# Kernel optimization log

Hardware: AMD Instinct MI355X
Metric: run time of the kernel (lower is better)

The kernel has to match this reference:

```python
import jax, jax.numpy as jnp
import numpy as np

N = 100000   # nodes
E = 500000   # edges
IN = 256     # in_dim
H = 256      # mlp_hidden = gnn_hidden = out_hidden
R = 3        # num_relations
EPS = 1e-5   # BatchNorm eps


def _bn(x, g, b, m, v):
    # eval-mode BatchNorm1d with running stats (m, v)
    return (x - m) * g / jnp.sqrt(v + EPS) + b


def _rel_agg(feat_src, agg_idx, etype, n, r):
    # per-(node, relation) segment sum and count in one fused segment reduce
    sid = agg_idx * r + etype                                   # (E,)
    sums = jax.ops.segment_sum(feat_src, sid, num_segments=n * r).reshape(n, r, -1)
    cnt = jax.ops.segment_sum(jnp.ones(feat_src.shape[:1], feat_src.dtype), sid,
                              num_segments=n * r).reshape(n, r, 1)
    return sums, cnt


def _scre(x, row, col, etype, r):
    # x - mean over active relations of per-relation neighbor means (aggregated at row)
    n = x.shape[0]
    sums, cnt = _rel_agg(x[col], row, etype, n, r)
    means = sums / jnp.maximum(cnt, 1.0)                        # (n, r, f)
    rel_count = jnp.maximum(jnp.sum(jnp.minimum(cnt, 1.0), axis=1), 1.0)  # (n, 1)
    return x - jnp.sum(means, axis=1) / rel_count


def _rgcn(x, row, col, etype, w_rel, w_root, bias, r):
    # PyG RGCNConv (aggr='mean'): per-relation mean of source feats at target + root + bias
    n = x.shape[0]
    sums, cnt = _rel_agg(x[row], col, etype, n, r)
    means = sums / jnp.maximum(cnt, 1.0)                        # (n, r, f)
    return jnp.einsum('nrf,rfo->no', means, w_rel) + x @ w_root + bias


def _forward(x, edge_index, edge_type,
             mlp_w1, mlp_b1, mbn1_g, mbn1_b, mbn1_m, mbn1_v,
             mlp_w2, mlp_b2, mbn2_g, mbn2_b, mbn2_m, mbn2_v,
             r1_wrel, r1_wroot, r1_b, gbn1_g, gbn1_b, gbn1_m, gbn1_v,
             r2_wrel, r2_wroot, r2_b, gbn2_g, gbn2_b, gbn2_m, gbn2_v,
             out_w, out_b):
    row, col = edge_index[0], edge_index[1]
    # MLP branch (dropout off in eval)
    z = jax.nn.relu(_bn(x @ mlp_w1 + mlp_b1, mbn1_g, mbn1_b, mbn1_m, mbn1_v))
    z_mlp = jax.nn.relu(_bn(z @ mlp_w2 + mlp_b2, mbn2_g, mbn2_b, mbn2_m, mbn2_v))
    h = _scre(x, row, col, edge_type, R)
    z = jax.nn.relu(_bn(_rgcn(h, row, col, edge_type, r1_wrel, r1_wroot, r1_b, R),
                        gbn1_g, gbn1_b, gbn1_m, gbn1_v))
    z_gnn = jax.nn.relu(_bn(_rgcn(z, row, col, edge_type, r2_wrel, r2_wroot, r2_b, R),
                            gbn2_g, gbn2_b, gbn2_m, gbn2_v))
    z = jnp.concatenate([z_mlp, z_gnn], axis=-1)                # (N, 2H)
    return (z @ out_w + out_b)[:, 0]                            # logits (N,)


def setup_inputs() -> dict:
    key = jax.random.key(0)
    ks = jax.random.split(key, 16)

    def w(k, shape):
        return jax.random.normal(k, shape, jnp.float32) * 0.05

    inp = {
        'x': jax.random.normal(ks[0], (N, IN), jnp.float32),
        'edge_index': jax.random.randint(ks[1], (2, E), 0, N),
        'edge_type': jax.random.randint(ks[2], (E,), 0, R),
        # MLP branch
        'mlp_w1': w(ks[3], (IN, H)), 'mlp_b1': jnp.zeros((H,), jnp.float32),
        'mbn1_g': jnp.ones((H,), jnp.float32), 'mbn1_b': jnp.zeros((H,), jnp.float32),
        'mbn1_m': 0.01 * jax.random.normal(ks[4], (H,), jnp.float32),
        'mbn1_v': 1.0 + 0.1 * jax.random.uniform(ks[5], (H,), jnp.float32),
        'mlp_w2': w(ks[6], (H, H)), 'mlp_b2': jnp.zeros((H,), jnp.float32),
        'mbn2_g': jnp.ones((H,), jnp.float32), 'mbn2_b': jnp.zeros((H,), jnp.float32),
        'mbn2_m': 0.01 * jax.random.normal(ks[7], (H,), jnp.float32),
        'mbn2_v': 1.0 + 0.1 * jax.random.uniform(ks[8], (H,), jnp.float32),
        # RGCN layer 1
        'r1_wrel': w(ks[9], (R, IN, H)), 'r1_wroot': w(ks[10], (IN, H)),
        'r1_b': jnp.zeros((H,), jnp.float32),
        'gbn1_g': jnp.ones((H,), jnp.float32), 'gbn1_b': jnp.zeros((H,), jnp.float32),
        'gbn1_m': 0.01 * jax.random.normal(ks[11], (H,), jnp.float32),
        'gbn1_v': 1.0 + 0.1 * jax.random.uniform(ks[12], (H,), jnp.float32),
        # RGCN layer 2
        'r2_wrel': w(ks[13], (R, H, H)), 'r2_wroot': w(ks[14], (H, H)),
        'r2_b': jnp.zeros((H,), jnp.float32),
        'gbn2_g': jnp.ones((H,), jnp.float32), 'gbn2_b': jnp.zeros((H,), jnp.float32),
        'gbn2_m': 0.01 * jax.random.normal(ks[15], (H,), jnp.float32),
        'gbn2_v': 1.0 + 0.1 * jax.random.uniform(jax.random.fold_in(key, 99), (H,), jnp.float32),
        # output head (proj_head does not affect returned logits; omitted)
        'out_w': 0.05 * jax.random.normal(jax.random.fold_in(key, 100), (2 * H, 1), jnp.float32),
        'out_b': jnp.zeros((1,), jnp.float32),
    }
    return inp


def reference(x, edge_index, edge_type,
              mlp_w1, mlp_b1, mbn1_g, mbn1_b, mbn1_m, mbn1_v,
              mlp_w2, mlp_b2, mbn2_g, mbn2_b, mbn2_m, mbn2_v,
              r1_wrel, r1_wroot, r1_b, gbn1_g, gbn1_b, gbn1_m, gbn1_v,
              r2_wrel, r2_wroot, r2_b, gbn2_g, gbn2_b, gbn2_m, gbn2_v,
              out_w, out_b):
    return _forward(x, edge_index, edge_type,
                    mlp_w1, mlp_b1, mbn1_g, mbn1_b, mbn1_m, mbn1_v,
                    mlp_w2, mlp_b2, mbn2_g, mbn2_b, mbn2_m, mbn2_v,
                    r1_wrel, r1_wroot, r1_b, gbn1_g, gbn1_b, gbn1_m, gbn1_v,
                    r2_wrel, r2_wroot, r2_b, gbn2_g, gbn2_b, gbn2_m, gbn2_v,
                    out_w, out_b)
```

## Files before the change

### kernel.cpp

```cpp
#include <hip/hip_runtime.h>

#define BN_EPS 1e-5f

typedef unsigned short u16;
typedef short bf16x8 __attribute__((ext_vector_type(8)));
typedef float f32x4 __attribute__((ext_vector_type(4)));

__device__ __forceinline__ float bf2f(u16 u) {
    return __uint_as_float(((unsigned)u) << 16);
}
__device__ __forceinline__ u16 f2bf(float f) {
    unsigned u = __float_as_uint(f);
    u += 0x7FFFu + ((u >> 16) & 1u);
    return (u16)(u >> 16);
}

__global__ __launch_bounds__(256) void k_count(const int* __restrict__ ei,
                                               const int* __restrict__ et,
                                               int* __restrict__ cntR,
                                               int* __restrict__ cntRT,
                                               int* __restrict__ cntCT, int E) {
    int e = blockIdx.x * 256 + threadIdx.x;
    if (e >= E) return;
    int r = ei[e], c = ei[E + e], t = et[e];
    atomicAdd(cntR + r, 1);
    atomicAdd(cntRT + (size_t)r * 3 + t, 1);
    atomicAdd(cntCT + (size_t)c * 3 + t, 1);
}

__global__ __launch_bounds__(256) void k_scales(const int* __restrict__ cntRT,
                                                float* __restrict__ sc_r, int N) {
    int n = blockIdx.x * 256 + threadIdx.x;
    if (n >= N) return;
    int c0 = cntRT[n * 3 + 0], c1 = cntRT[n * 3 + 1], c2 = cntRT[n * 3 + 2];
    float relc = (float)((c0 > 0) + (c1 > 0) + (c2 > 0));
    if (relc < 1.f) relc = 1.f;
    sc_r[n * 3 + 0] = c0 > 0 ? 1.f / ((float)c0 * relc) : 0.f;
    sc_r[n * 3 + 1] = c1 > 0 ? 1.f / ((float)c1 * relc) : 0.f;
    sc_r[n * 3 + 2] = c2 > 0 ? 1.f / ((float)c2 * relc) : 0.f;
}

__global__ __launch_bounds__(256) void k_scan1(const int* __restrict__ in,
                                               int* __restrict__ out,
                                               int* __restrict__ bsums, int n) {
    __shared__ int sh[256];
    int t = threadIdx.x, base = blockIdx.x * 2048 + t * 8;
    int v[8];
    int s = 0;
#pragma unroll
    for (int j = 0; j < 8; ++j) {
        int idx = base + j;
        v[j] = idx < n ? in[idx] : 0;
        s += v[j];
    }
    sh[t] = s;
    __syncthreads();
    for (int off = 1; off < 256; off <<= 1) {
        int val = (t >= off) ? sh[t - off] : 0;
        __syncthreads();
        sh[t] += val;
        __syncthreads();
    }
    int run = sh[t] - s;
    if (t == 255) bsums[blockIdx.x] = sh[255];
#pragma unroll
    for (int j = 0; j < 8; ++j) {
        int idx = base + j;
        if (idx < n) out[idx] = run;
        run += v[j];
    }
}
__global__ __launch_bounds__(256) void k_scan2(int* __restrict__ bsums, int nb) {
    __shared__ int sh[256];
    int t = threadIdx.x;
    int v = t < nb ? bsums[t] : 0;
    sh[t] = v;
    __syncthreads();
    for (int off = 1; off < 256; off <<= 1) {
        int val = (t >= off) ? sh[t - off] : 0;
        __syncthreads();
        sh[t] += val;
        __syncthreads();
    }
    if (t < nb) bsums[t] = sh[t] - v;
}
__global__ __launch_bounds__(256) void k_scan3(int* __restrict__ out,
                                               const int* __restrict__ bsums, int n) {
    int i = blockIdx.x * 2048 + threadIdx.x * 8;
    int add = bsums[blockIdx.x];
#pragma unroll
    for (int j = 0; j < 8; ++j)
        if (i + j < n) out[i + j] += add;
}

__global__ __launch_bounds__(256) void k_scatter(const int* __restrict__ ei,
                                                 const int* __restrict__ et,
                                                 const float* __restrict__ sc_r,
                                                 const int* __restrict__ offR,
                                                 int* __restrict__ fillR,
                                                 int* __restrict__ idxR,
                                                 float* __restrict__ coefR,
                                                 const int* __restrict__ offC,
                                                 int* __restrict__ fillC,
                                                 int* __restrict__ idxC, int E) {
    int e = blockIdx.x * 256 + threadIdx.x;
    if (e >= E) return;
    int r = ei[e], c = ei[E + e], t = et[e];
    int pR = offR[r] + atomicAdd(fillR + r, 1);
    idxR[pR] = c;
    coefR[pR] = sc_r[(size_t)r * 3 + t];
    int key = c * 3 + t;
    int pC = offC[key] + atomicAdd(fillC + key, 1);
    idxC[pC] = r;
}

__global__ __launch_bounds__(256) void k_scre_gather(const float* __restrict__ x,
                                                     const int* __restrict__ idxR,
                                                     const float* __restrict__ coefR,
                                                     const int* __restrict__ offR,
                                                     const int* __restrict__ cntR,
                                                     u16* __restrict__ h, int N) {
    int node = blockIdx.x * 4 + (threadIdx.x >> 6);
    if (node >= N) return;
    int lane = threadIdx.x & 63;
    int start = offR[node], len = cntR[node];
    float4 acc = make_float4(0.f, 0.f, 0.f, 0.f);
    for (int i = 0; i < len; ++i) {
        int c = idxR[start + i];
        float s = coefR[start + i];
        float4 v = *reinterpret_cast<const float4*>(x + (size_t)c * 256 + lane * 4);
        acc.x += s * v.x;
        acc.y += s * v.y;
        acc.z += s * v.z;
        acc.w += s * v.w;
    }
    float4 xv = *reinterpret_cast<const float4*>(x + (size_t)node * 256 + lane * 4);
    ushort4 o;
    o.x = f2bf(xv.x - acc.x);
    o.y = f2bf(xv.y - acc.y);
    o.z = f2bf(xv.z - acc.z);
    o.w = f2bf(xv.w - acc.w);
    *reinterpret_cast<ushort4*>(h + (size_t)node * 256 + lane * 4) = o;
}

__global__ __launch_bounds__(256) void k_rgcn_gather(const u16* __restrict__ src,
                                                     const int* __restrict__ idxC,
                                                     const int* __restrict__ offC,
                                                     const int* __restrict__ cntC,
                                                     u16* __restrict__ means,
                                                     int s0, int s1) {
    int seg = s0 + blockIdx.x * 4 + (threadIdx.x >> 6);
    if (seg >= s1) return;
    int lane = threadIdx.x & 63;
    int start = offC[seg], len = cntC[seg];
    float4 acc = make_float4(0.f, 0.f, 0.f, 0.f);
    for (int i = 0; i < len; ++i) {
        int r = idxC[start + i];
        ushort4 v = *reinterpret_cast<const ushort4*>(src + (size_t)r * 256 + lane * 4);
        acc.x += bf2f(v.x);
        acc.y += bf2f(v.y);
        acc.z += bf2f(v.z);
        acc.w += bf2f(v.w);
    }
    float inv = len > 0 ? 1.f / (float)len : 0.f;
    ushort4 o;
    o.x = f2bf(acc.x * inv);
    o.y = f2bf(acc.y * inv);
    o.z = f2bf(acc.z * inv);
    o.w = f2bf(acc.w * inv);
    *reinterpret_cast<ushort4*>(means + (size_t)(seg - s0) * 256 + lane * 4) = o;
}

__global__ __launch_bounds__(256) void k_wt(const float* __restrict__ W,
                                            u16* __restrict__ Wt, int K) {
    __shared__ float tile[32][33];
    int kb = blockIdx.x * 32, nb = blockIdx.y * 32;
    int tx = threadIdx.x & 31, ty = threadIdx.x >> 5;
#pragma unroll
    for (int j = 0; j < 4; ++j) {
        int k = kb + ty + j * 8;
        tile[ty + j * 8][tx] = W[(size_t)k * 256 + nb + tx];
    }
    __syncthreads();
#pragma unroll
    for (int j = 0; j < 4; ++j) {
        int n = nb + ty + j * 8;
        Wt[(size_t)n * K + kb + tx] = f2bf(tile[tx][ty + j * 8]);
    }
}

#define LDK 40

template <int A1_F32>
__global__ __launch_bounds__(256) void k_gemm_mfma(
    const void* __restrict__ A1v, int K1, const u16* __restrict__ W1t,
    const u16* __restrict__ A2, int K2, const u16* __restrict__ W2t,
    const float* __restrict__ bias,
    const float* __restrict__ bng, const float* __restrict__ bnb,
    const float* __restrict__ bnm, const float* __restrict__ bnv,
    u16* __restrict__ out, int M) {
    __shared__ u16 Asm[128 * LDK];
    __shared__ u16 Bsm[128 * LDK];
    const int tid = threadIdx.x;
    const int lane = tid & 63;
    const int wid = tid >> 6;
    const int wr = wid >> 1, wc = wid & 1;
    const int m0 = blockIdx.x * 128, n0 = blockIdx.y * 128;
    const int frow = lane & 15, fk = (lane >> 4) * 8;

    f32x4 acc[4][4] = {};

    for (int pass = 0; pass < 2; ++pass) {
        const int K = pass ? K2 : K1;
        if (K == 0) continue;
        const u16* Wt = pass ? W2t : W1t;
        for (int k0 = 0; k0 < K; k0 += 32) {
            __syncthreads();
#pragma unroll
            for (int j = 0; j < 2; ++j) {
                int q = tid + 256 * j;
                int row = q >> 2, kc = (q & 3) * 8;
                int gm = m0 + row;
                bf16x8 av = {};
                if (gm < M) {
                    if (pass == 0 && A1_F32) {
                        const float* p = (const float*)A1v + (size_t)gm * K + k0 + kc;
#pragma unroll
                        for (int e2 = 0; e2 < 8; ++e2)
                            ((u16*)&av)[e2] = f2bf(p[e2]);
                    } else {
                        const u16* Ab = pass ? A2 : (const u16*)A1v;
                        av = *reinterpret_cast<const bf16x8*>(Ab + (size_t)gm * K + k0 + kc);
                    }
                }
                *reinterpret_cast<bf16x8*>(&Asm[row * LDK + kc]) = av;
                bf16x8 wv = *reinterpret_cast<const bf16x8*>(Wt + (size_t)(n0 + row) * K + k0 + kc);
                *reinterpret_cast<bf16x8*>(&Bsm[row * LDK + kc]) = wv;
            }
            __syncthreads();
            bf16x8 af[4], bf[4];
#pragma unroll
            for (int i = 0; i < 4; ++i) {
                af[i] = *reinterpret_cast<const bf16x8*>(&Asm[(wr * 64 + i * 16 + frow) * LDK + fk]);
                bf[i] = *reinterpret_cast<const bf16x8*>(&Bsm[(wc * 64 + i * 16 + frow) * LDK + fk]);
            }
#pragma unroll
            for (int i = 0; i < 4; ++i)
#pragma unroll
                for (int j2 = 0; j2 < 4; ++j2)
                    acc[i][j2] = __builtin_amdgcn_mfma_f32_16x16x32_bf16(af[i], bf[j2], acc[i][j2], 0, 0, 0);
        }
    }

    const int crow = (lane >> 4) * 4;
#pragma unroll
    for (int fj = 0; fj < 4; ++fj) {
        int col = n0 + wc * 64 + fj * 16 + frow;
        float g = bng[col] * rsqrtf(bnv[col] + BN_EPS);
        float be = bnb[col] + (bias[col] - bnm[col]) * g;
#pragma unroll
        for (int fi = 0; fi < 4; ++fi) {
#pragma unroll
            for (int j = 0; j < 4; ++j) {
                int row = m0 + wr * 64 + fi * 16 + crow + j;
                if (row < M) {
                    float y = acc[fi][fj][j] * g + be;
                    out[(size_t)row * 256 + col] = f2bf(y > 0.f ? y : 0.f);
                }
            }
        }
    }
}

__global__ __launch_bounds__(256) void k_head(const u16* __restrict__ zm,
                                              const u16* __restrict__ zg,
                                              const float* __restrict__ ow,
                                              const float* __restrict__ ob,
                                              float* __restrict__ out, int N) {
    int n = blockIdx.x * 4 + (threadIdx.x >> 6);
    if (n >= N) return;
    int lane = threadIdx.x & 63;
    ushort4 a = *reinterpret_cast<const ushort4*>(zm + (size_t)n * 256 + lane * 4);
    float4 w = *reinterpret_cast<const float4*>(ow + lane * 4);
    float s = bf2f(a.x) * w.x + bf2f(a.y) * w.y + bf2f(a.z) * w.z + bf2f(a.w) * w.w;
    ushort4 b = *reinterpret_cast<const ushort4*>(zg + (size_t)n * 256 + lane * 4);
    float4 w2 = *reinterpret_cast<const float4*>(ow + 256 + lane * 4);
    s += bf2f(b.x) * w2.x + bf2f(b.y) * w2.y + bf2f(b.z) * w2.z + bf2f(b.w) * w2.w;
#pragma unroll
    for (int off = 32; off > 0; off >>= 1) s += __shfl_down(s, off);
    if (lane == 0) out[n] = s + ob[0];
}

static inline size_t alignup(size_t x) { return (x + 255) & ~(size_t)255; }

extern "C" void kernel_launch(void* const* d_in, const int* in_sizes, int n_in,
                              void* d_out, int out_size, void* d_ws, size_t ws_size,
                              hipStream_t stream) {
    const float* x = (const float*)d_in[0];
    const int* ei = (const int*)d_in[1];
    const int* et = (const int*)d_in[2];
    const float* mlp_w1 = (const float*)d_in[3];
    const float* mlp_b1 = (const float*)d_in[4];
    const float* mbn1_g = (const float*)d_in[5];
    const float* mbn1_b = (const float*)d_in[6];
    const float* mbn1_m = (const float*)d_in[7];
    const float* mbn1_v = (const float*)d_in[8];
    const float* mlp_w2 = (const float*)d_in[9];
    const float* mlp_b2 = (const float*)d_in[10];
    const float* mbn2_g = (const float*)d_in[11];
    const float* mbn2_b = (const float*)d_in[12];
    const float* mbn2_m = (const float*)d_in[13];
    const float* mbn2_v = (const float*)d_in[14];
    const float* r1_wrel = (const float*)d_in[15];
    const float* r1_wroot = (const float*)d_in[16];
    const float* r1_b = (const float*)d_in[17];
    const float* gbn1_g = (const float*)d_in[18];
    const float* gbn1_b = (const float*)d_in[19];
    const float* gbn1_m = (const float*)d_in[20];
    const float* gbn1_v = (const float*)d_in[21];
    const float* r2_wrel = (const float*)d_in[22];
    const float* r2_wroot = (const float*)d_in[23];
    const float* r2_b = (const float*)d_in[24];
    const float* gbn2_g = (const float*)d_in[25];
    const float* gbn2_b = (const float*)d_in[26];
    const float* gbn2_m = (const float*)d_in[27];
    const float* gbn2_v = (const float*)d_in[28];
    const float* out_w = (const float*)d_in[29];
    const float* out_b = (const float*)d_in[30];

    const int N = in_sizes[0] / 256;
    const int E = in_sizes[2];

    size_t off = 0;
    auto take = [&](size_t bytes) {
        size_t o = off;
        off = alignup(off + bytes);
        return o;
    };
    char* base = (char*)d_ws;
    size_t zeroOff = take((size_t)N * 11 * 4);
    int* cntR = (int*)(base + zeroOff);
    int* cntRT = cntR + N;
    int* cntCT = cntRT + (size_t)N * 3;
    int* fillR = cntCT + (size_t)N * 3;
    int* fillC = fillR + N;
    int* offR = (int*)(base + take((size_t)N * 4));
    int* offC = (int*)(base + take((size_t)N * 3 * 4));
    int* bsums = (int*)(base + take(256 * 4));
    float* sc_r = (float*)(base + take((size_t)N * 3 * 4));
    int* idxR = (int*)(base + take((size_t)E * 4));
    float* coefR = (float*)(base + take((size_t)E * 4));
    int* idxC = (int*)(base + take((size_t)E * 4));
    u16* w1t = (u16*)(base + take((size_t)256 * 256 * 2));
    u16* w2t = (u16*)(base + take((size_t)256 * 256 * 2));
    u16* r1relt = (u16*)(base + take((size_t)256 * 768 * 2));
    u16* r1roott = (u16*)(base + take((size_t)256 * 256 * 2));
    u16* r2relt = (u16*)(base + take((size_t)256 * 768 * 2));
    u16* r2roott = (u16*)(base + take((size_t)256 * 256 * 2));
    u16* regA = (u16*)(base + take((size_t)N * 256 * 2));
    u16* regB = (u16*)(base + take((size_t)N * 256 * 2));
    u16* regC = (u16*)(base + take((size_t)N * 256 * 2));
    size_t chunkOff = off;
    size_t avail = (ws_size > chunkOff) ? ws_size - chunkOff : 0;
    size_t ncap = avail / ((size_t)768 * 2);
    if (ncap < 2048) {
        hipMemsetAsync(d_out, 0, (size_t)out_size * 4, stream);
        return;
    }
    int Nc = (int)((ncap < (size_t)N) ? ncap : (size_t)N);
    int nch = (N + Nc - 1) / Nc;
    Nc = (N + nch - 1) / nch;
    u16* CH = (u16*)(base + chunkOff);

    hipMemsetAsync(cntR, 0, (size_t)N * 11 * 4, stream);
    k_count<<<(E + 255) / 256, 256, 0, stream>>>(ei, et, cntR, cntRT, cntCT, E);
    k_scales<<<(N + 255) / 256, 256, 0, stream>>>(cntRT, sc_r, N);
    {
        int n1 = N, nb1 = (n1 + 2047) / 2048;
        k_scan1<<<nb1, 256, 0, stream>>>(cntR, offR, bsums, n1);
        k_scan2<<<1, 256, 0, stream>>>(bsums, nb1);
        k_scan3<<<nb1, 256, 0, stream>>>(offR, bsums, n1);
        int n2 = N * 3, nb2 = (n2 + 2047) / 2048;
        k_scan1<<<nb2, 256, 0, stream>>>(cntCT, offC, bsums, n2);
        k_scan2<<<1, 256, 0, stream>>>(bsums, nb2);
        k_scan3<<<nb2, 256, 0, stream>>>(offC, bsums, n2);
    }
    k_scatter<<<(E + 255) / 256, 256, 0, stream>>>(ei, et, sc_r, offR, fillR, idxR,
                                                   coefR, offC, fillC, idxC, E);

    k_wt<<<dim3(8, 8), 256, 0, stream>>>(mlp_w1, w1t, 256);
    k_wt<<<dim3(8, 8), 256, 0, stream>>>(mlp_w2, w2t, 256);
    k_wt<<<dim3(24, 8), 256, 0, stream>>>(r1_wrel, r1relt, 768);
    k_wt<<<dim3(8, 8), 256, 0, stream>>>(r1_wroot, r1roott, 256);
    k_wt<<<dim3(24, 8), 256, 0, stream>>>(r2_wrel, r2relt, 768);
    k_wt<<<dim3(8, 8), 256, 0, stream>>>(r2_wroot, r2roott, 256);

    {
        dim3 g((N + 127) / 128, 2);
        k_gemm_mfma<1><<<g, 256, 0, stream>>>(x, 256, w1t, nullptr, 0, nullptr,
                                              mlp_b1, mbn1_g, mbn1_b, mbn1_m, mbn1_v,
                                              regA, N);
        k_gemm_mfma<0><<<g, 256, 0, stream>>>(regA, 256, w2t, nullptr, 0, nullptr,
                                              mlp_b2, mbn2_g, mbn2_b, mbn2_m, mbn2_v,
                                              regB, N);
    }

    k_scre_gather<<<(N + 3) / 4, 256, 0, stream>>>(x, idxR, coefR, offR, cntR, regA, N);

    for (int ch = 0; ch < nch; ++ch) {
        int n0 = ch * Nc;
        int n1 = (n0 + Nc < N) ? n0 + Nc : N;
        int Mc = n1 - n0;
        int s0 = n0 * 3, s1 = n1 * 3;
        k_rgcn_gather<<<(s1 - s0 + 3) / 4, 256, 0, stream>>>(regA, idxC, offC, cntCT,
                                                             CH, s0, s1);
        dim3 g((Mc + 127) / 128, 2);
        k_gemm_mfma<0><<<g, 256, 0, stream>>>(CH, 768, r1relt,
                                              regA + (size_t)n0 * 256, 256, r1roott,
                                              r1_b, gbn1_g, gbn1_b, gbn1_m, gbn1_v,
                                              regC + (size_t)n0 * 256, Mc);
    }

    for (int ch = 0; ch < nch; ++ch) {
        int n0 = ch * Nc;
        int n1 = (n0 + Nc < N) ? n0 + Nc : N;
        int Mc = n1 - n0;
        int s0 = n0 * 3, s1 = n1 * 3;
        k_rgcn_gather<<<(s1 - s0 + 3) / 4, 256, 0, stream>>>(regC, idxC, offC, cntCT,
                                                             CH, s0, s1);
        dim3 g((Mc + 127) / 128, 2);
        k_gemm_mfma<0><<<g, 256, 0, stream>>>(CH, 768, r2relt,
                                              regC + (size_t)n0 * 256, 256, r2roott,
                                              r2_b, gbn2_g, gbn2_b, gbn2_m, gbn2_v,
                                              regA + (size_t)n0 * 256, Mc);
    }

    k_head<<<(N + 3) / 4, 256, 0, stream>>>(regB, regA, out_w, out_b, (float*)d_out, N);
}
```

Before: 1.038 ms.

## Widen GEMM tile to full 256 columns with double-buffered register prefetch

The MFMA GEMM now computes all 256 output columns per block instead of splitting N across two blocks, so the A tile (including the fp32-to-bf16 converted input) is loaded only once. The two-pass K loop is flattened into a single loop with register prefetch and double-buffered LDS to overlap global loads with MFMA work. The RGCN gather moves to 32 lanes per segment with 8-element bf16 vector loads. This raises accumulator registers (4x8 fragments) and LDS use, which may lower occupancy, and halves the number of GEMM blocks.

Measured after the change: 1.017 ms. Within noise of the previous version (-1.9%).

```diff
diff --git a/kernel.cpp b/kernel.cpp
--- a/kernel.cpp
+++ b/kernel.cpp
@@ -149,26 +149,22 @@
                                                      const int* __restrict__ cntC,
                                                      u16* __restrict__ means,
                                                      int s0, int s1) {
-    int seg = s0 + blockIdx.x * 4 + (threadIdx.x >> 6);
+    int seg = s0 + blockIdx.x * 8 + (threadIdx.x >> 5);
     if (seg >= s1) return;
-    int lane = threadIdx.x & 63;
+    int lane = threadIdx.x & 31;
     int start = offC[seg], len = cntC[seg];
-    float4 acc = make_float4(0.f, 0.f, 0.f, 0.f);
+    float acc[8] = {};
     for (int i = 0; i < len; ++i) {
         int r = idxC[start + i];
-        ushort4 v = *reinterpret_cast<const ushort4*>(src + (size_t)r * 256 + lane * 4);
-        acc.x += bf2f(v.x);
-        acc.y += bf2f(v.y);
-        acc.z += bf2f(v.z);
-        acc.w += bf2f(v.w);
+        bf16x8 v = *reinterpret_cast<const bf16x8*>(src + (size_t)r * 256 + lane * 8);
+#pragma unroll
+        for (int e = 0; e < 8; ++e) acc[e] += bf2f(((u16*)&v)[e]);
     }
     float inv = len > 0 ? 1.f / (float)len : 0.f;
-    ushort4 o;
-    o.x = f2bf(acc.x * inv);
-    o.y = f2bf(acc.y * inv);
-    o.z = f2bf(acc.z * inv);
-    o.w = f2bf(acc.w * inv);
-    *reinterpret_cast<ushort4*>(means + (size_t)(seg - s0) * 256 + lane * 4) = o;
+    bf16x8 o;
+#pragma unroll
+    for (int e = 0; e < 8; ++e) ((u16*)&o)[e] = f2bf(acc[e] * inv);
+    *reinterpret_cast<bf16x8*>(means + (size_t)(seg - s0) * 256 + lane * 8) = o;
 }
 
 __global__ __launch_bounds__(256) void k_wt(const float* __restrict__ W,
@@ -190,6 +186,7 @@
 }
 
 #define LDK 40
+#define BM 128
 
 template <int A1_F32>
 __global__ __launch_bounds__(256) void k_gemm_mfma(
@@ -199,63 +196,103 @@
     const float* __restrict__ bng, const float* __restrict__ bnb,
     const float* __restrict__ bnm, const float* __restrict__ bnv,
     u16* __restrict__ out, int M) {
-    __shared__ u16 Asm[128 * LDK];
-    __shared__ u16 Bsm[128 * LDK];
+    __shared__ u16 Asm[2][BM * LDK];
+    __shared__ u16 Bsm[2][256 * LDK];
     const int tid = threadIdx.x;
     const int lane = tid & 63;
     const int wid = tid >> 6;
     const int wr = wid >> 1, wc = wid & 1;
-    const int m0 = blockIdx.x * 128, n0 = blockIdx.y * 128;
+    const int m0 = blockIdx.x * BM;
     const int frow = lane & 15, fk = (lane >> 4) * 8;
-
-    f32x4 acc[4][4] = {};
-
-    for (int pass = 0; pass < 2; ++pass) {
-        const int K = pass ? K2 : K1;
-        if (K == 0) continue;
-        const u16* Wt = pass ? W2t : W1t;
-        for (int k0 = 0; k0 < K; k0 += 32) {
-            __syncthreads();
-#pragma unroll
-            for (int j = 0; j < 2; ++j) {
-                int q = tid + 256 * j;
-                int row = q >> 2, kc = (q & 3) * 8;
-                int gm = m0 + row;
-                bf16x8 av = {};
+    const int arow = tid >> 2;
+    const int achunk = (tid & 3) * 8;
+
+    const int nsteps = (K1 + K2) >> 5;
+
+    f32x4 acc[4][8] = {};
+    bf16x8 pa[2], pb[4];
+
+    {
+        const int kg = 0;
+#pragma unroll
+        for (int s = 0; s < 2; ++s) {
+            int gm = m0 + arow + 64 * s;
+            bf16x8 v = {};
+            if (gm < M) {
+                if (A1_F32) {
+                    const float* p = (const float*)A1v + (size_t)gm * K1 + kg + achunk;
+#pragma unroll
+                    for (int e = 0; e < 8; ++e) ((u16*)&v)[e] = f2bf(p[e]);
+                } else {
+                    v = *reinterpret_cast<const bf16x8*>((const u16*)A1v + (size_t)gm * K1 + kg + achunk);
+                }
+            }
+            pa[s] = v;
+        }
+#pragma unroll
+        for (int s = 0; s < 4; ++s)
+            pb[s] = *reinterpret_cast<const bf16x8*>(W1t + (size_t)(arow + 64 * s) * K1 + kg + achunk);
+    }
+
+    int cur = 0;
+    for (int ks = 0; ks < nsteps; ++ks) {
+#pragma unroll
+        for (int s = 0; s < 2; ++s)
+            *reinterpret_cast<bf16x8*>(&Asm[cur][(arow + 64 * s) * LDK + achunk]) = pa[s];
+#pragma unroll
+        for (int s = 0; s < 4; ++s)
+            *reinterpret_cast<bf16x8*>(&Bsm[cur][(arow + 64 * s) * LDK + achunk]) = pb[s];
+        __syncthreads();
+
+        if (ks + 1 < nsteps) {
+            const int kg = (ks + 1) * 32;
+#pragma unroll
+            for (int s = 0; s < 2; ++s) {
+                int gm = m0 + arow + 64 * s;
+                bf16x8 v = {};
                 if (gm < M) {
-                    if (pass == 0 && A1_F32) {
-                        const float* p = (const float*)A1v + (size_t)gm * K + k0 + kc;
-#pragma unroll
-                        for (int e2 = 0; e2 < 8; ++e2)
-                            ((u16*)&av)[e2] = f2bf(p[e2]);
+                    if (kg < K1) {
+                        if (A1_F32) {
+                            const float* p = (const float*)A1v + (size_t)gm * K1 + kg + achunk;
+#pragma unroll
+                            for (int e = 0; e < 8; ++e) ((u16*)&v)[e] = f2bf(p[e]);
+                        } else {
+                            v = *reinterpret_cast<const bf16x8*>((const u16*)A1v + (size_t)gm * K1 + kg + achunk);
+                        }
                     } else {
-                        const u16* Ab = pass ? A2 : (const u16*)A1v;
-                        av = *reinterpret_cast<const bf16x8*>(Ab + (size_t)gm * K + k0 + kc);
+                        v = *reinterpret_cast<const bf16x8*>(A2 + (size_t)gm * K2 + (kg - K1) + achunk);
                     }
                 }
-                *reinterpret_cast<bf16x8*>(&Asm[row * LDK + kc]) = av;
-                bf16x8 wv = *reinterpret_cast<const bf16x8*>(Wt + (size_t)(n0 + row) * K + k0 + kc);
-                *reinterpret_cast<bf16x8*>(&Bsm[row * LDK + kc]) = wv;
+                pa[s] = v;
             }
-            __syncthreads();
-            bf16x8 af[4], bf[4];
-#pragma unroll
-            for (int i = 0; i < 4; ++i) {
-                af[i] = *reinterpret_cast<const bf16x8*>(&Asm[(wr * 64 + i * 16 + frow) * LDK + fk]);
-                bf[i] = *reinterpret_cast<const bf16x8*>(&Bsm[(wc * 64 + i * 16 + frow) * LDK + fk]);
+#pragma unroll
+            for (int s = 0; s < 4; ++s) {
+                int row = arow + 64 * s;
+                if (kg < K1)
+                    pb[s] = *reinterpret_cast<const bf16x8*>(W1t + (size_t)row * K1 + kg + achunk);
+                else
+                    pb[s] = *reinterpret_cast<const bf16x8*>(W2t + (size_t)row * K2 + (kg - K1) + achunk);
             }
+        }
+
+        bf16x8 af[4];
+#pragma unroll
+        for (int i = 0; i < 4; ++i)
+            af[i] = *reinterpret_cast<const bf16x8*>(&Asm[cur][(wr * 64 + i * 16 + frow) * LDK + fk]);
+#pragma unroll
+        for (int j = 0; j < 8; ++j) {
+            bf16x8 bfr = *reinterpret_cast<const bf16x8*>(&Bsm[cur][(wc * 128 + j * 16 + frow) * LDK + fk]);
 #pragma unroll
             for (int i = 0; i < 4; ++i)
-#pragma unroll
-                for (int j2 = 0; j2 < 4; ++j2)
-                    acc[i][j2] = __builtin_amdgcn_mfma_f32_16x16x32_bf16(af[i], bf[j2], acc[i][j2], 0, 0, 0);
+                acc[i][j] = __builtin_amdgcn_mfma_f32_16x16x32_bf16(af[i], bfr, acc[i][j], 0, 0, 0);
         }
+        cur ^= 1;
     }
 
     const int crow = (lane >> 4) * 4;
 #pragma unroll
-    for (int fj = 0; fj < 4; ++fj) {
-        int col = n0 + wc * 64 + fj * 16 + frow;
+    for (int fj = 0; fj < 8; ++fj) {
+        int col = wc * 128 + fj * 16 + frow;
         float g = bng[col] * rsqrtf(bnv[col] + BN_EPS);
         float be = bnb[col] + (bias[col] - bnm[col]) * g;
 #pragma unroll
@@ -396,7 +433,7 @@
     k_wt<<<dim3(8, 8), 256, 0, stream>>>(r2_wroot, r2roott, 256);
 
     {
-        dim3 g((N + 127) / 128, 2);
+        dim3 g((N + 127) / 128);
         k_gemm_mfma<1><<<g, 256, 0, stream>>>(x, 256, w1t, nullptr, 0, nullptr,
                                               mlp_b1, mbn1_g, mbn1_b, mbn1_m, mbn1_v,
                                               regA, N);
@@ -412,9 +449,9 @@
         int n1 = (n0 + Nc < N) ? n0 + Nc : N;
         int Mc = n1 - n0;
         int s0 = n0 * 3, s1 = n1 * 3;
-        k_rgcn_gather<<<(s1 - s0 + 3) / 4, 256, 0, stream>>>(regA, idxC, offC, cntCT,
+        k_rgcn_gather<<<(s1 - s0 + 7) / 8, 256, 0, stream>>>(regA, idxC, offC, cntCT,
                                                              CH, s0, s1);
-        dim3 g((Mc + 127) / 128, 2);
+        dim3 g((Mc + 127) / 128);
         k_gemm_mfma<0><<<g, 256, 0, stream>>>(CH, 768, r1relt,
                                               regA + (size_t)n0 * 256, 256, r1roott,
                                               r1_b, gbn1_g, gbn1_b, gbn1_m, gbn1_v,
@@ -426,9 +463,9 @@
         int n1 = (n0 + Nc < N) ? n0 + Nc : N;
         int Mc = n1 - n0;
         int s0 = n0 * 3, s1 = n1 * 3;
-        k_rgcn_gather<<<(s1 - s0 + 3) / 4, 256, 0, stream>>>(regC, idxC, offC, cntCT,
+        k_rgcn_gather<<<(s1 - s0 + 7) / 8, 256, 0, stream>>>(regC, idxC, offC, cntCT,
                                                              CH, s0, s1);
-        dim3 g((Mc + 127) / 128, 2);
+        dim3 g((Mc + 127) / 128);
         k_gemm_mfma<0><<<g, 256, 0, stream>>>(CH, 768, r2relt,
                                               regC + (size_t)n0 * 256, 256, r2roott,
                                               r2_b, gbn2_g, gbn2_b, gbn2_m, gbn2_v,
```

## Pre-convert x to bf16, widen gather vectors, and hoist GEMM global loads

Applied to the files above, without the earlier changes.

Adds a kernel that converts x to bf16 once. The first MLP GEMM and the SCRE gather then read bf16 instead of fp32, which halves the gather traffic on x. Both gather kernels switch to 32 lanes per row with 8-element (16-byte) loads and handle 8 rows per block. The GEMM now issues its global loads into registers before the barrier and writes them to LDS afterwards, so load latency overlaps the wait. SCRE now works on bf16-rounded x, which may change accuracy slightly, and the extra pass and buffer add memory traffic and workspace.

New measurement: 879.6 us. -15.2%, faster.

```diff
diff --git a/kernel.cpp b/kernel.cpp
--- a/kernel.cpp
+++ b/kernel.cpp
@@ -13,6 +13,24 @@
     unsigned u = __float_as_uint(f);
     u += 0x7FFFu + ((u >> 16) & 1u);
     return (u16)(u >> 16);
+}
+
+__global__ __launch_bounds__(256) void k_xbf(const float* __restrict__ x,
+                                             u16* __restrict__ xb, int n8) {
+    int i = blockIdx.x * 256 + threadIdx.x;
+    if (i >= n8) return;
+    const float4 a = *reinterpret_cast<const float4*>(x + (size_t)i * 8);
+    const float4 b = *reinterpret_cast<const float4*>(x + (size_t)i * 8 + 4);
+    bf16x8 o;
+    ((u16*)&o)[0] = f2bf(a.x);
+    ((u16*)&o)[1] = f2bf(a.y);
+    ((u16*)&o)[2] = f2bf(a.z);
+    ((u16*)&o)[3] = f2bf(a.w);
+    ((u16*)&o)[4] = f2bf(b.x);
+    ((u16*)&o)[5] = f2bf(b.y);
+    ((u16*)&o)[6] = f2bf(b.z);
+    ((u16*)&o)[7] = f2bf(b.w);
+    *reinterpret_cast<bf16x8*>(xb + (size_t)i * 8) = o;
 }
 
 __global__ __launch_bounds__(256) void k_count(const int* __restrict__ ei,
@@ -114,33 +132,29 @@
     idxC[pC] = r;
 }
 
-__global__ __launch_bounds__(256) void k_scre_gather(const float* __restrict__ x,
+__global__ __launch_bounds__(256) void k_scre_gather(const u16* __restrict__ xb,
                                                      const int* __restrict__ idxR,
                                                      const float* __restrict__ coefR,
                                                      const int* __restrict__ offR,
                                                      const int* __restrict__ cntR,
                                                      u16* __restrict__ h, int N) {
-    int node = blockIdx.x * 4 + (threadIdx.x >> 6);
+    int node = blockIdx.x * 8 + (threadIdx.x >> 5);
     if (node >= N) return;
-    int lane = threadIdx.x & 63;
+    int lane = threadIdx.x & 31;
     int start = offR[node], len = cntR[node];
-    float4 acc = make_float4(0.f, 0.f, 0.f, 0.f);
+    float acc[8] = {};
     for (int i = 0; i < len; ++i) {
         int c = idxR[start + i];
         float s = coefR[start + i];
-        float4 v = *reinterpret_cast<const float4*>(x + (size_t)c * 256 + lane * 4);
-        acc.x += s * v.x;
-        acc.y += s * v.y;
-        acc.z += s * v.z;
-        acc.w += s * v.w;
-    }
-    float4 xv = *reinterpret_cast<const float4*>(x + (size_t)node * 256 + lane * 4);
-    ushort4 o;
-    o.x = f2bf(xv.x - acc.x);
-    o.y = f2bf(xv.y - acc.y);
-    o.z = f2bf(xv.z - acc.z);
-    o.w = f2bf(xv.w - acc.w);
-    *reinterpret_cast<ushort4*>(h + (size_t)node * 256 + lane * 4) = o;
+        bf16x8 v = *reinterpret_cast<const bf16x8*>(xb + (size_t)c * 256 + lane * 8);
+#pragma unroll
+        for (int e = 0; e < 8; ++e) acc[e] += s * bf2f(((u16*)&v)[e]);
+    }
+    bf16x8 xv = *reinterpret_cast<const bf16x8*>(xb + (size_t)node * 256 + lane * 8);
+    bf16x8 o;
+#pragma unroll
+    for (int e = 0; e < 8; ++e) ((u16*)&o)[e] = f2bf(bf2f(((u16*)&xv)[e]) - acc[e]);
+    *reinterpret_cast<bf16x8*>(h + (size_t)node * 256 + lane * 8) = o;
 }
 
 __global__ __launch_bounds__(256) void k_rgcn_gather(const u16* __restrict__ src,
@@ -149,26 +163,22 @@
                                                      const int* __restrict__ cntC,
                                                      u16* __restrict__ means,
                                                      int s0, int s1) {
-    int seg = s0 + blockIdx.x * 4 + (threadIdx.x >> 6);
+    int seg = s0 + blockIdx.x * 8 + (threadIdx.x >> 5);
     if (seg >= s1) return;
-    int lane = threadIdx.x & 63;
+    int lane = threadIdx.x & 31;
     int start = offC[seg], len = cntC[seg];
-    float4 acc = make_float4(0.f, 0.f, 0.f, 0.f);
+    float acc[8] = {};
     for (int i = 0; i < len; ++i) {
         int r = idxC[start + i];
-        ushort4 v = *reinterpret_cast<const ushort4*>(src + (size_t)r * 256 + lane * 4);
-        acc.x += bf2f(v.x);
-        acc.y += bf2f(v.y);
-        acc.z += bf2f(v.z);
-        acc.w += bf2f(v.w);
+        bf16x8 v = *reinterpret_cast<const bf16x8*>(src + (size_t)r * 256 + lane * 8);
+#pragma unroll
+        for (int e = 0; e < 8; ++e) acc[e] += bf2f(((u16*)&v)[e]);
     }
     float inv = len > 0 ? 1.f / (float)len : 0.f;
-    ushort4 o;
-    o.x = f2bf(acc.x * inv);
-    o.y = f2bf(acc.y * inv);
-    o.z = f2bf(acc.z * inv);
-    o.w = f2bf(acc.w * inv);
-    *reinterpret_cast<ushort4*>(means + (size_t)(seg - s0) * 256 + lane * 4) = o;
+    bf16x8 o;
+#pragma unroll
+    for (int e = 0; e < 8; ++e) ((u16*)&o)[e] = f2bf(acc[e] * inv);
+    *reinterpret_cast<bf16x8*>(means + (size_t)(seg - s0) * 256 + lane * 8) = o;
 }
 
 __global__ __launch_bounds__(256) void k_wt(const float* __restrict__ W,
@@ -191,9 +201,8 @@
 
 #define LDK 40
 
-template <int A1_F32>
 __global__ __launch_bounds__(256) void k_gemm_mfma(
-    const void* __restrict__ A1v, int K1, const u16* __restrict__ W1t,
+    const u16* __restrict__ A1, int K1, const u16* __restrict__ W1t,
     const u16* __restrict__ A2, int K2, const u16* __restrict__ W2t,
     const float* __restrict__ bias,
     const float* __restrict__ bng, const float* __restrict__ bnb,
@@ -213,42 +222,41 @@
     for (int pass = 0; pass < 2; ++pass) {
         const int K = pass ? K2 : K1;
         if (K == 0) continue;
+        const u16* A = pass ? A2 : A1;
         const u16* Wt = pass ? W2t : W1t;
         for (int k0 = 0; k0 < K; k0 += 32) {
-            __syncthreads();
+            bf16x8 av[2], wv[2];
 #pragma unroll
             for (int j = 0; j < 2; ++j) {
                 int q = tid + 256 * j;
                 int row = q >> 2, kc = (q & 3) * 8;
                 int gm = m0 + row;
-                bf16x8 av = {};
-                if (gm < M) {
-                    if (pass == 0 && A1_F32) {
-                        const float* p = (const float*)A1v + (size_t)gm * K + k0 + kc;
-#pragma unroll
-                        for (int e2 = 0; e2 < 8; ++e2)
-                            ((u16*)&av)[e2] = f2bf(p[e2]);
-                    } else {
-                        const u16* Ab = pass ? A2 : (const u16*)A1v;
-                        av = *reinterpret_cast<const bf16x8*>(Ab + (size_t)gm * K + k0 + kc);
-                    }
-                }
-                *reinterpret_cast<bf16x8*>(&Asm[row * LDK + kc]) = av;
-                bf16x8 wv = *reinterpret_cast<const bf16x8*>(Wt + (size_t)(n0 + row) * K + k0 + kc);
-                *reinterpret_cast<bf16x8*>(&Bsm[row * LDK + kc]) = wv;
+                bf16x8 v = {};
+                if (gm < M)
+                    v = *reinterpret_cast<const bf16x8*>(A + (size_t)gm * K + k0 + kc);
+                av[j] = v;
+                wv[j] = *reinterpret_cast<const bf16x8*>(Wt + (size_t)(n0 + row) * K + k0 + kc);
             }
             __syncthreads();
-            bf16x8 af[4], bf[4];
+#pragma unroll
+            for (int j = 0; j < 2; ++j) {
+                int q = tid + 256 * j;
+                int row = q >> 2, kc = (q & 3) * 8;
+                *reinterpret_cast<bf16x8*>(&Asm[row * LDK + kc]) = av[j];
+                *reinterpret_cast<bf16x8*>(&Bsm[row * LDK + kc]) = wv[j];
+            }
+            __syncthreads();
+            bf16x8 af[4], bfr[4];
 #pragma unroll
             for (int i = 0; i < 4; ++i) {
                 af[i] = *reinterpret_cast<const bf16x8*>(&Asm[(wr * 64 + i * 16 + frow) * LDK + fk]);
-                bf[i] = *reinterpret_cast<const bf16x8*>(&Bsm[(wc * 64 + i * 16 + frow) * LDK + fk]);
+                bfr[i] = *reinterpret_cast<const bf16x8*>(&Bsm[(wc * 64 + i * 16 + frow) * LDK + fk]);
             }
 #pragma unroll
             for (int i = 0; i < 4; ++i)
 #pragma unroll
                 for (int j2 = 0; j2 < 4; ++j2)
-                    acc[i][j2] = __builtin_amdgcn_mfma_f32_16x16x32_bf16(af[i], bf[j2], acc[i][j2], 0, 0, 0);
+                    acc[i][j2] = __builtin_amdgcn_mfma_f32_16x16x32_bf16(af[i], bfr[j2], acc[i][j2], 0, 0, 0);
         }
     }
 
@@ -357,6 +365,7 @@
     u16* r1roott = (u16*)(base + take((size_t)256 * 256 * 2));
     u16* r2relt = (u16*)(base + take((size_t)256 * 768 * 2));
     u16* r2roott = (u16*)(base + take((size_t)256 * 256 * 2));
+    u16* xb = (u16*)(base + take((size_t)N * 256 * 2));
     u16* regA = (u16*)(base + take((size_t)N * 256 * 2));
     u16* regB = (u16*)(base + take((size_t)N * 256 * 2));
     u16* regC = (u16*)(base + take((size_t)N * 256 * 2));
@@ -371,6 +380,8 @@
     int nch = (N + Nc - 1) / Nc;
     Nc = (N + nch - 1) / nch;
     u16* CH = (u16*)(base + chunkOff);
+
+    k_xbf<<<(N * 32 + 255) / 256, 256, 0, stream>>>(x, xb, N * 32);
 
     hipMemsetAsync(cntR, 0, (size_t)N * 11 * 4, stream);
     k_count<<<(E + 255) / 256, 256, 0, stream>>>(ei, et, cntR, cntRT, cntCT, E);
@@ -397,28 +408,28 @@
 
     {
         dim3 g((N + 127) / 128, 2);
-        k_gemm_mfma<1><<<g, 256, 0, stream>>>(x, 256, w1t, nullptr, 0, nullptr,
-                                              mlp_b1, mbn1_g, mbn1_b, mbn1_m, mbn1_v,
-                                              regA, N);
-        k_gemm_mfma<0><<<g, 256, 0, stream>>>(regA, 256, w2t, nullptr, 0, nullptr,
-                                              mlp_b2, mbn2_g, mbn2_b, mbn2_m, mbn2_v,
-                                              regB, N);
-    }
-
-    k_scre_gather<<<(N + 3) / 4, 256, 0, stream>>>(x, idxR, coefR, offR, cntR, regA, N);
+        k_gemm_mfma<<<g, 256, 0, stream>>>(xb, 256, w1t, nullptr, 0, nullptr,
+                                           mlp_b1, mbn1_g, mbn1_b, mbn1_m, mbn1_v,
+                                           regA, N);
+        k_gemm_mfma<<<g, 256, 0, stream>>>(regA, 256, w2t, nullptr, 0, nullptr,
+                                           mlp_b2, mbn2_g, mbn2_b, mbn2_m, mbn2_v,
+                                           regB, N);
+    }
+
+    k_scre_gather<<<(N + 7) / 8, 256, 0, stream>>>(xb, idxR, coefR, offR, cntR, regA, N);
 
     for (int ch = 0; ch < nch; ++ch) {
         int n0 = ch * Nc;
         int n1 = (n0 + Nc < N) ? n0 + Nc : N;
         int Mc = n1 - n0;
         int s0 = n0 * 3, s1 = n1 * 3;
-        k_rgcn_gather<<<(s1 - s0 + 3) / 4, 256, 0, stream>>>(regA, idxC, offC, cntCT,
+        k_rgcn_gather<<<(s1 - s0 + 7) / 8, 256, 0, stream>>>(regA, idxC, offC, cntCT,
                                                              CH, s0, s1);
         dim3 g((Mc + 127) / 128, 2);
-        k_gemm_mfma<0><<<g, 256, 0, stream>>>(CH, 768, r1relt,
-                                              regA + (size_t)n0 * 256, 256, r1roott,
-                                              r1_b, gbn1_g, gbn1_b, gbn1_m, gbn1_v,
-                                              regC + (size_t)n0 * 256, Mc);
+        k_gemm_mfma<<<g, 256, 0, stream>>>(CH, 768, r1relt,
+                                           regA + (size_t)n0 * 256, 256, r1roott,
+                                           r1_b, gbn1_g, gbn1_b, gbn1_m, gbn1_v,
+                                           regC + (size_t)n0 * 256, Mc);
     }
 
     for (int ch = 0; ch < nch; ++ch) {
@@ -426,13 +437,13 @@
         int n1 = (n0 + Nc < N) ? n0 + Nc : N;
         int Mc = n1 - n0;
         int s0 = n0 * 3, s1 = n1 * 3;
-        k_rgcn_gather<<<(s1 - s0 + 3) / 4, 256, 0, stream>>>(regC, idxC, offC, cntCT,
+        k_rgcn_gather<<<(s1 - s0 + 7) / 8, 256, 0, stream>>>(regC, idxC, offC, cntCT,
                                                              CH, s0, s1);
         dim3 g((Mc + 127) / 128, 2);
-        k_gemm_mfma<0><<<g, 256, 0, stream>>>(CH, 768, r2relt,
-                                              regC + (size_t)n0 * 256, 256, r2roott,
-                                              r2_b, gbn2_g, gbn2_b, gbn2_m, gbn2_v,
-                                              regA + (size_t)n0 * 256, Mc);
+        k_gemm_mfma<<<g, 256, 0, stream>>>(CH, 768, r2relt,
+                                           regC + (size_t)n0 * 256, 256, r2roott,
+                                           r2_b, gbn2_g, gbn2_b, gbn2_m, gbn2_v,
+                                           regA + (size_t)n0 * 256, Mc);
     }
 
     k_head<<<(N + 3) / 4, 256, 0, stream>>>(regB, regA, out_w, out_b, (float*)d_out, N);
```
